# Kernel optimization log

Measured on AMD Instinct MI355X. Metric: run time of the kernel, lower is better.

Reference implementation:

```python
import jax, jax.numpy as jnp
import numpy as np

B, L, D = 1, 256, 256
H, DK, R = 8, 32, 2
EPS = 1e-6


def _proj_ode(x, t, W, b, r):
    """Stand-in for ODELinear/InterpLinear: linear projection of x broadcast
    over a second time index with r exponential time-decay coefficients.
    x: [B,L,D], t: [B,L] -> [B,L,L,r,D_out]"""
    base = x @ W.T + b                                  # [B,L,Do]
    dt = jnp.abs(t[:, :, None] - t[:, None, :])         # [B,L,L]
    steps = jnp.linspace(0.0, 1.0, r, dtype=x.dtype)    # [r]
    coef = jnp.exp(-dt[:, :, :, None] * steps)          # [B,L,L,r]
    return coef[..., None] * base[:, None, :, None, :]  # [B,L,L,r,Do]


def _layer_norm(x, g, b):
    mu = x.mean(-1, keepdims=True)
    var = ((x - mu) ** 2).mean(-1, keepdims=True)
    return (x - mu) * jax.lax.rsqrt(var + EPS) * g + b


def setup_inputs() -> dict:
    key = jax.random.key(0)
    ks = jax.random.split(key, 12)
    s = 1.0 / np.sqrt(D)
    return {
        "q": jax.random.normal(ks[0], (B, L, D), jnp.float32),
        "k": jax.random.normal(ks[1], (B, L, D), jnp.float32),
        "v": jax.random.normal(ks[2], (B, L, D), jnp.float32),
        "t": jax.random.uniform(ks[3], (B, L), jnp.float32),
        "Wq": jax.random.normal(ks[4], (D, D), jnp.float32) * s,
        "bq": jnp.zeros((D,), jnp.float32),
        "Wk": jax.random.normal(ks[5], (D, D), jnp.float32) * s,
        "bk": jnp.zeros((D,), jnp.float32),
        "Wv": jax.random.normal(ks[6], (D, D), jnp.float32) * s,
        "bv": jnp.zeros((D,), jnp.float32),
        "fc_w": jax.random.normal(ks[7], (D, D), jnp.float32) * s,
        "fc_b": jnp.zeros((D,), jnp.float32),
        "ln_g": jnp.ones((D,), jnp.float32),
        "ln_b": jnp.zeros((D,), jnp.float32),
    }


def reference(q, k, v, t, Wq, bq, Wk, bk, Wv, bv, fc_w, fc_b, ln_g, ln_b):
    temp = DK ** 0.5
    residual = q
    qn = _layer_norm(q, ln_g, ln_b)  # normalize_before=True (only q)

    # [B,L,L,R,D] -> [B,L,L,R,H,DK] -> [B,H,L,L,R,DK]
    def to6(x):
        return x.reshape(B, L, L, R, H, DK).transpose(0, 4, 1, 2, 3, 5)

    qp = to6(_proj_ode(qn, t, Wq, bq, R))
    kp = to6(_proj_ode(k, t, Wk, bk, R))
    vp = to6(_proj_ode(v, t, Wv, bv, R))

    # attn = (q/temp * k).sum(-1).sum(-1): multiply-reduce over (R, DK), no matmul
    attn = jnp.einsum('bhijrd,bhijrd->bhij', qp, kp) / temp
    attn = jax.nn.softmax(attn, axis=-1)  # dropout=0 (eval)

    vs = vp.sum(axis=4)                                   # reduce R: [B,H,L,L,DK]
    out = jnp.einsum('bhij,bhijd->bhid', attn, vs)        # reduce second L
    out = out.transpose(0, 2, 1, 3).reshape(B, L, H * DK)
    out = out @ fc_w.T + fc_b
    out = out + residual
    return (out, attn)
```

## Files before the change

kernel.cpp:

```cpp
#include <hip/hip_runtime.h>
#include <math.h>


#define INV_TEMP 0.17677669529663687f

__device__ __forceinline__ void gemm_panel(
    const float* __restrict__ X, const float* __restrict__ W,
    const float* __restrict__ bias, const float* __restrict__ ln_g,
    const float* __restrict__ ln_b, float* __restrict__ out, const int mode) {
  __shared__ float As[256][36];
  __shared__ float Bs[256][36];
  __shared__ float Red[4][32][36];
  const int t = threadIdx.x;
  const int j0 = blockIdx.y << 5, o0 = blockIdx.x << 5;
  const int lr = t >> 3;
  const int cg = (t & 7) << 2;
  float4 xa[8], wb[8];
#pragma unroll
  for (int u = 0; u < 8; ++u) {
    xa[u] = *(const float4*)(X + ((j0 + lr) << 8) + (u << 5) + cg);
    wb[u] = *(const float4*)(W + ((o0 + lr) << 8) + (u << 5) + cg);
  }
  if (mode == 0) {
    float s = 0.f, s2 = 0.f;
#pragma unroll
    for (int u = 0; u < 8; ++u) {
      s  += xa[u].x + xa[u].y + xa[u].z + xa[u].w;
      s2 += xa[u].x * xa[u].x + xa[u].y * xa[u].y +
            xa[u].z * xa[u].z + xa[u].w * xa[u].w;
    }
#pragma unroll
    for (int off = 1; off < 8; off <<= 1) {
      s  += __shfl_xor(s, off);
      s2 += __shfl_xor(s2, off);
    }
    const float mu = s * 0.00390625f;
    const float rs = rsqrtf(s2 * 0.00390625f - mu * mu + 1e-6f);
#pragma unroll
    for (int u = 0; u < 8; ++u) {
      const float4 gv = *(const float4*)(ln_g + (u << 5) + cg);
      const float4 bv = *(const float4*)(ln_b + (u << 5) + cg);
      xa[u].x = (xa[u].x - mu) * rs * gv.x + bv.x;
      xa[u].y = (xa[u].y - mu) * rs * gv.y + bv.y;
      xa[u].z = (xa[u].z - mu) * rs * gv.z + bv.z;
      xa[u].w = (xa[u].w - mu) * rs * gv.w + bv.w;
    }
  }
#pragma unroll
  for (int u = 0; u < 8; ++u) {
    const int c = (u << 5) + cg;
    As[c + 0][lr] = xa[u].x; As[c + 1][lr] = xa[u].y;
    As[c + 2][lr] = xa[u].z; As[c + 3][lr] = xa[u].w;
    Bs[c + 0][lr] = wb[u].x; Bs[c + 1][lr] = wb[u].y;
    Bs[c + 2][lr] = wb[u].z; Bs[c + 3][lr] = wb[u].w;
  }
  __syncthreads();

  const int w = t >> 6, lane = t & 63;
  const int jb = (lane >> 3) << 2;
  const int ob = (lane & 7) << 2;
  const int kbase = w << 6;
  float acc[4][4] = {{0.f}};
#pragma unroll 8
  for (int kk = 0; kk < 64; ++kk) {
    const float4 av = *(const float4*)&As[kbase + kk][jb];
    const float4 bv = *(const float4*)&Bs[kbase + kk][ob];
    acc[0][0] = fmaf(av.x, bv.x, acc[0][0]);
    acc[0][1] = fmaf(av.x, bv.y, acc[0][1]);
    acc[0][2] = fmaf(av.x, bv.z, acc[0][2]);
    acc[0][3] = fmaf(av.x, bv.w, acc[0][3]);
    acc[1][0] = fmaf(av.y, bv.x, acc[1][0]);
    acc[1][1] = fmaf(av.y, bv.y, acc[1][1]);
    acc[1][2] = fmaf(av.y, bv.z, acc[1][2]);
    acc[1][3] = fmaf(av.y, bv.w, acc[1][3]);
    acc[2][0] = fmaf(av.z, bv.x, acc[2][0]);
    acc[2][1] = fmaf(av.z, bv.y, acc[2][1]);
    acc[2][2] = fmaf(av.z, bv.z, acc[2][2]);
    acc[2][3] = fmaf(av.z, bv.w, acc[2][3]);
    acc[3][0] = fmaf(av.w, bv.x, acc[3][0]);
    acc[3][1] = fmaf(av.w, bv.y, acc[3][1]);
    acc[3][2] = fmaf(av.w, bv.z, acc[3][2]);
    acc[3][3] = fmaf(av.w, bv.w, acc[3][3]);
  }
#pragma unroll
  for (int r = 0; r < 4; ++r)
    *(float4*)&Red[w][jb + r][ob] =
        make_float4(acc[r][0], acc[r][1], acc[r][2], acc[r][3]);
  __syncthreads();

  const int j = t >> 3, o4 = (t & 7) << 2;
  const float4 s0 = *(const float4*)&Red[0][j][o4];
  const float4 s1 = *(const float4*)&Red[1][j][o4];
  const float4 s2 = *(const float4*)&Red[2][j][o4];
  const float4 s3 = *(const float4*)&Red[3][j][o4];
  const float4 bv4 = *(const float4*)(bias + o0 + o4);
  float4 rs4;
  rs4.x = (s0.x + s1.x) + (s2.x + s3.x) + bv4.x;
  rs4.y = (s0.y + s1.y) + (s2.y + s3.y) + bv4.y;
  rs4.z = (s0.z + s1.z) + (s2.z + s3.z) + bv4.z;
  rs4.w = (s0.w + s1.w) + (s2.w + s3.w) + bv4.w;
  const int gj = j0 + j, go = o0 + o4;
  if (mode <= 1) {
    out[((go + 0) << 8) + gj] = rs4.x;
    out[((go + 1) << 8) + gj] = rs4.y;
    out[((go + 2) << 8) + gj] = rs4.z;
    out[((go + 3) << 8) + gj] = rs4.w;
  } else {
    *(float4*)(out + (gj << 8) + go) = rs4;
  }
}

__global__ __launch_bounds__(256) void mha_proj_gemm3(
    const float* __restrict__ q, const float* __restrict__ kin,
    const float* __restrict__ vin, const float* __restrict__ Wq,
    const float* __restrict__ bq, const float* __restrict__ Wk,
    const float* __restrict__ bk, const float* __restrict__ Wv,
    const float* __restrict__ bv, const float* __restrict__ ln_g,
    const float* __restrict__ ln_b, const float* __restrict__ fc_w,
    float* __restrict__ baseQT, float* __restrict__ baseKT,
    float* __restrict__ baseV, float* __restrict__ fc_wT,
    float* __restrict__ outz) {
  const int z = blockIdx.z;
  const int gid = ((z << 6) + (blockIdx.y << 3) + blockIdx.x) * 256 +
                  threadIdx.x;
  if (gid < 16384)
    ((float4*)outz)[gid] = make_float4(0.f, 0.f, 0.f, 0.f);
  {
    const int e = gid << 1;
    if (e < 65536) {
      const float2 v = *(const float2*)(fc_w + e);
      const int o = e >> 8, d = e & 255;
      fc_wT[(d << 8) + o] = v.x;
      fc_wT[((d + 1 < 256 ? d + 1 : d - 255) << 8) +
            (d + 1 < 256 ? o : o + 1)] = v.y;
    }
  }
  if (z == 0)
    gemm_panel(q, Wq, bq, ln_g, ln_b, baseQT, 0);
  else if (z == 1)
    gemm_panel(kin, Wk, bk, nullptr, nullptr, baseKT, 1);
  else
    gemm_panel(vin, Wv, bv, nullptr, nullptr, baseV, 2);
}

__global__ __launch_bounds__(512) void mha_attn_fc(
    const float* __restrict__ baseQT, const float* __restrict__ baseKT,
    const float* __restrict__ baseV, const float* __restrict__ tt,
    const float* __restrict__ fc_wT, const float* __restrict__ fc_b,
    const float* __restrict__ qres, float* __restrict__ attn_out,
    float* __restrict__ out) {
  const int h = blockIdx.y;
  const int i0 = blockIdx.x << 3;
  const int t = threadIdx.x;
  __shared__ float s_lds[256];
  __shared__ float P[8][256];
  __shared__ float ctx_lds[8][32];
  if (t < 256) {
    const float* qc = baseQT + (h << 13) + t;
    const float* kc = baseKT + (h << 13) + t;
    float acc = 0.f;
#pragma unroll
    for (int dk = 0; dk < 32; ++dk)
      acc = fmaf(qc[dk << 8], kc[dk << 8], acc);
    s_lds[t] = acc * INV_TEMP;
  }
  __syncthreads();

  const int w = t >> 6, lane = t & 63;
  const int i = i0 + w;
  const float ti = tt[i];
  const float4 tj = ((const float4*)tt)[lane];
  const float4 sv = ((const float4*)s_lds)[lane];
  const float e0 = __expf(-fabsf(ti - tj.x));
  const float e1 = __expf(-fabsf(ti - tj.y));
  const float e2 = __expf(-fabsf(ti - tj.z));
  const float e3 = __expf(-fabsf(ti - tj.w));
  const float sc0 = (1.f + e0 * e0) * sv.x;
  const float sc1 = (1.f + e1 * e1) * sv.y;
  const float sc2 = (1.f + e2 * e2) * sv.z;
  const float sc3 = (1.f + e3 * e3) * sv.w;
  float m = fmaxf(fmaxf(sc0, sc1), fmaxf(sc2, sc3));
#pragma unroll
  for (int off = 32; off; off >>= 1) m = fmaxf(m, __shfl_xor(m, off));
  float p0 = __expf(sc0 - m), p1 = __expf(sc1 - m);
  float p2 = __expf(sc2 - m), p3 = __expf(sc3 - m);
  float s = p0 + p1 + p2 + p3;
#pragma unroll
  for (int off = 32; off; off >>= 1) s += __shfl_xor(s, off);
  const float rinv = 1.f / s;
  p0 *= rinv; p1 *= rinv; p2 *= rinv; p3 *= rinv;
  ((float4*)(attn_out + (((h << 8) + i) << 8)))[lane] =
      make_float4(p0, p1, p2, p3);
  ((float4*)P[w])[lane] = make_float4(p0 * (1.f + e0), p1 * (1.f + e1),
                                      p2 * (1.f + e2), p3 * (1.f + e3));

  const int dk = lane & 31, half = lane >> 5;
  const float* Pr = P[w] + (half << 7);
  const float* Vp = baseV + (h << 5) + dk + (half << 15);
  float a0 = 0.f, a1 = 0.f, a2 = 0.f, a3 = 0.f;
#pragma unroll 4
  for (int jj = 0; jj < 128; jj += 4) {
    a0 = fmaf(Pr[jj + 0], Vp[(jj + 0) << 8], a0);
    a1 = fmaf(Pr[jj + 1], Vp[(jj + 1) << 8], a1);
    a2 = fmaf(Pr[jj + 2], Vp[(jj + 2) << 8], a2);
    a3 = fmaf(Pr[jj + 3], Vp[(jj + 3) << 8], a3);
  }
  float acc = (a0 + a1) + (a2 + a3);
  acc += __shfl_xor(acc, 32);
  if (half == 0) ctx_lds[w][dk] = acc;
  __syncthreads();

  const int oq = lane << 2;
  float4 c4[8];
#pragma unroll
  for (int u = 0; u < 8; ++u)
    c4[u] = *(const float4*)&ctx_lds[w][u << 2];
  const float* wt = fc_wT + (h << 13) + oq;
  float4 acc4 = make_float4(0.f, 0.f, 0.f, 0.f);
#pragma unroll
  for (int u = 0; u < 8; ++u) {
    const float4 cc = c4[u];
    const float4 w0 = *(const float4*)(wt + ((u << 2) + 0 << 8));
    const float4 w1 = *(const float4*)(wt + ((u << 2) + 1 << 8));
    const float4 w2 = *(const float4*)(wt + ((u << 2) + 2 << 8));
    const float4 w3 = *(const float4*)(wt + ((u << 2) + 3 << 8));
    acc4.x = fmaf(cc.x, w0.x, fmaf(cc.y, w1.x, fmaf(cc.z, w2.x, fmaf(cc.w, w3.x, acc4.x))));
    acc4.y = fmaf(cc.x, w0.y, fmaf(cc.y, w1.y, fmaf(cc.z, w2.y, fmaf(cc.w, w3.y, acc4.y))));
    acc4.z = fmaf(cc.x, w0.z, fmaf(cc.y, w1.z, fmaf(cc.z, w2.z, fmaf(cc.w, w3.z, acc4.z))));
    acc4.w = fmaf(cc.x, w0.w, fmaf(cc.y, w1.w, fmaf(cc.z, w2.w, fmaf(cc.w, w3.w, acc4.w))));
  }
  if (h == 0) {
    const float4 bb = *(const float4*)(fc_b + oq);
    const float4 rr = *(const float4*)(qres + (i << 8) + oq);
    acc4.x += bb.x + rr.x; acc4.y += bb.y + rr.y;
    acc4.z += bb.z + rr.z; acc4.w += bb.w + rr.w;
  }
  float* op = out + (i << 8) + oq;
  unsafeAtomicAdd(op + 0, acc4.x);
  unsafeAtomicAdd(op + 1, acc4.y);
  unsafeAtomicAdd(op + 2, acc4.z);
  unsafeAtomicAdd(op + 3, acc4.w);
}

extern "C" void kernel_launch(void* const* d_in, const int* in_sizes, int n_in,
                              void* d_out, int out_size, void* d_ws,
                              size_t ws_size, hipStream_t stream) {
  const float* q    = (const float*)d_in[0];
  const float* kin  = (const float*)d_in[1];
  const float* vin  = (const float*)d_in[2];
  const float* tt   = (const float*)d_in[3];
  const float* Wq   = (const float*)d_in[4];
  const float* bq   = (const float*)d_in[5];
  const float* Wk   = (const float*)d_in[6];
  const float* bk   = (const float*)d_in[7];
  const float* Wv   = (const float*)d_in[8];
  const float* bv   = (const float*)d_in[9];
  const float* fc_w = (const float*)d_in[10];
  const float* fc_b = (const float*)d_in[11];
  const float* ln_g = (const float*)d_in[12];
  const float* ln_b = (const float*)d_in[13];

  float* out  = (float*)d_out;
  float* attn = out + 65536;

  float* ws     = (float*)d_ws;
  float* baseQT = ws;
  float* baseKT = ws + 65536;
  float* baseV  = ws + 131072;
  float* fc_wT  = ws + 196608;

  hipLaunchKernelGGL(mha_proj_gemm3, dim3(8, 8, 3), dim3(256), 0, stream, q,
                     kin, vin, Wq, bq, Wk, bk, Wv, bv, ln_g, ln_b, fc_w,
                     baseQT, baseKT, baseV, fc_wT, out);
  hipLaunchKernelGGL(mha_attn_fc, dim3(32, 8), dim3(512), 0, stream, baseQT,
                     baseKT, baseV, tt, fc_wT, fc_b, q, attn, out);
}
```

Before: 103.1 us.

## Loop heads inside attention block and replace atomic FC accumulation with direct stores

The attention kernel now gives each block 4 query rows and loops over all 8 heads inside the block, instead of using one block per (head, 8-row) tile. Each block therefore holds the full 256-wide context per row and can finish the output projection with plain float4 stores. This removes the zero-initialisation of the output in the first kernel and the per-head atomic adds. The cost is only 64 blocks of 256 threads, so far fewer waves are in flight. Each block also recomputes the per-head score vectors for all 8 heads, and the head loop runs serially inside each block.

```diff
diff --git a/kernel.cpp b/kernel.cpp
--- a/kernel.cpp
+++ b/kernel.cpp
@@ -118,13 +118,10 @@
     const float* __restrict__ bv, const float* __restrict__ ln_g,
     const float* __restrict__ ln_b, const float* __restrict__ fc_w,
     float* __restrict__ baseQT, float* __restrict__ baseKT,
-    float* __restrict__ baseV, float* __restrict__ fc_wT,
-    float* __restrict__ outz) {
+    float* __restrict__ baseV, float* __restrict__ fc_wT) {
   const int z = blockIdx.z;
   const int gid = ((z << 6) + (blockIdx.y << 3) + blockIdx.x) * 256 +
                   threadIdx.x;
-  if (gid < 16384)
-    ((float4*)outz)[gid] = make_float4(0.f, 0.f, 0.f, 0.f);
   {
     const int e = gid << 1;
     if (e < 65536) {
@@ -143,26 +140,27 @@
     gemm_panel(vin, Wv, bv, nullptr, nullptr, baseV, 2);
 }
 
-__global__ __launch_bounds__(512) void mha_attn_fc(
+__global__ __launch_bounds__(256) void mha_attn_fc(
     const float* __restrict__ baseQT, const float* __restrict__ baseKT,
     const float* __restrict__ baseV, const float* __restrict__ tt,
     const float* __restrict__ fc_wT, const float* __restrict__ fc_b,
     const float* __restrict__ qres, float* __restrict__ attn_out,
     float* __restrict__ out) {
-  const int h = blockIdx.y;
-  const int i0 = blockIdx.x << 3;
+  const int i0 = blockIdx.x << 2;
   const int t = threadIdx.x;
-  __shared__ float s_lds[256];
-  __shared__ float P[8][256];
-  __shared__ float ctx_lds[8][32];
-  if (t < 256) {
+  __shared__ float s_lds[8][256];
+  __shared__ float P[4][256];
+  __shared__ float ctx_lds[4][256];
+
+#pragma unroll
+  for (int h = 0; h < 8; ++h) {
     const float* qc = baseQT + (h << 13) + t;
     const float* kc = baseKT + (h << 13) + t;
     float acc = 0.f;
 #pragma unroll
     for (int dk = 0; dk < 32; ++dk)
       acc = fmaf(qc[dk << 8], kc[dk << 8], acc);
-    s_lds[t] = acc * INV_TEMP;
+    s_lds[h][t] = acc * INV_TEMP;
   }
   __syncthreads();
 
@@ -170,76 +168,62 @@
   const int i = i0 + w;
   const float ti = tt[i];
   const float4 tj = ((const float4*)tt)[lane];
-  const float4 sv = ((const float4*)s_lds)[lane];
   const float e0 = __expf(-fabsf(ti - tj.x));
   const float e1 = __expf(-fabsf(ti - tj.y));
   const float e2 = __expf(-fabsf(ti - tj.z));
   const float e3 = __expf(-fabsf(ti - tj.w));
-  const float sc0 = (1.f + e0 * e0) * sv.x;
-  const float sc1 = (1.f + e1 * e1) * sv.y;
-  const float sc2 = (1.f + e2 * e2) * sv.z;
-  const float sc3 = (1.f + e3 * e3) * sv.w;
-  float m = fmaxf(fmaxf(sc0, sc1), fmaxf(sc2, sc3));
-#pragma unroll
-  for (int off = 32; off; off >>= 1) m = fmaxf(m, __shfl_xor(m, off));
-  float p0 = __expf(sc0 - m), p1 = __expf(sc1 - m);
-  float p2 = __expf(sc2 - m), p3 = __expf(sc3 - m);
-  float s = p0 + p1 + p2 + p3;
-#pragma unroll
-  for (int off = 32; off; off >>= 1) s += __shfl_xor(s, off);
-  const float rinv = 1.f / s;
-  p0 *= rinv; p1 *= rinv; p2 *= rinv; p3 *= rinv;
-  ((float4*)(attn_out + (((h << 8) + i) << 8)))[lane] =
-      make_float4(p0, p1, p2, p3);
-  ((float4*)P[w])[lane] = make_float4(p0 * (1.f + e0), p1 * (1.f + e1),
-                                      p2 * (1.f + e2), p3 * (1.f + e3));
-
+  const float f0 = 1.f + e0, f1 = 1.f + e1, f2 = 1.f + e2, f3 = 1.f + e3;
+  const float g0 = 1.f + e0 * e0, g1 = 1.f + e1 * e1;
+  const float g2 = 1.f + e2 * e2, g3 = 1.f + e3 * e3;
   const int dk = lane & 31, half = lane >> 5;
-  const float* Pr = P[w] + (half << 7);
-  const float* Vp = baseV + (h << 5) + dk + (half << 15);
-  float a0 = 0.f, a1 = 0.f, a2 = 0.f, a3 = 0.f;
+
+  for (int h = 0; h < 8; ++h) {
+    const float4 sv = ((const float4*)s_lds[h])[lane];
+    const float sc0 = g0 * sv.x, sc1 = g1 * sv.y;
+    const float sc2 = g2 * sv.z, sc3 = g3 * sv.w;
+    float m = fmaxf(fmaxf(sc0, sc1), fmaxf(sc2, sc3));
+#pragma unroll
+    for (int off = 32; off; off >>= 1) m = fmaxf(m, __shfl_xor(m, off));
+    float p0 = __expf(sc0 - m), p1 = __expf(sc1 - m);
+    float p2 = __expf(sc2 - m), p3 = __expf(sc3 - m);
+    float s = p0 + p1 + p2 + p3;
+#pragma unroll
+    for (int off = 32; off; off >>= 1) s += __shfl_xor(s, off);
+    const float rinv = 1.f / s;
+    p0 *= rinv; p1 *= rinv; p2 *= rinv; p3 *= rinv;
+    ((float4*)(attn_out + (((h << 8) + i) << 8)))[lane] =
+        make_float4(p0, p1, p2, p3);
+    ((float4*)P[w])[lane] =
+        make_float4(p0 * f0, p1 * f1, p2 * f2, p3 * f3);
+    const float* Pr = P[w] + (half << 7);
+    const float* Vp = baseV + (h << 5) + dk + (half << 15);
+    float a0 = 0.f, a1 = 0.f, a2 = 0.f, a3 = 0.f;
 #pragma unroll 4
-  for (int jj = 0; jj < 128; jj += 4) {
-    a0 = fmaf(Pr[jj + 0], Vp[(jj + 0) << 8], a0);
-    a1 = fmaf(Pr[jj + 1], Vp[(jj + 1) << 8], a1);
-    a2 = fmaf(Pr[jj + 2], Vp[(jj + 2) << 8], a2);
-    a3 = fmaf(Pr[jj + 3], Vp[(jj + 3) << 8], a3);
-  }
-  float acc = (a0 + a1) + (a2 + a3);
-  acc += __shfl_xor(acc, 32);
-  if (half == 0) ctx_lds[w][dk] = acc;
-  __syncthreads();
+    for (int jj = 0; jj < 128; jj += 4) {
+      a0 = fmaf(Pr[jj + 0], Vp[(jj + 0) << 8], a0);
+      a1 = fmaf(Pr[jj + 1], Vp[(jj + 1) << 8], a1);
+      a2 = fmaf(Pr[jj + 2], Vp[(jj + 2) << 8], a2);
+      a3 = fmaf(Pr[jj + 3], Vp[(jj + 3) << 8], a3);
+    }
+    float acc = (a0 + a1) + (a2 + a3);
+    acc += __shfl_xor(acc, 32);
+    if (half == 0) ctx_lds[w][(h << 5) + dk] = acc;
+  }
 
   const int oq = lane << 2;
-  float4 c4[8];
-#pragma unroll
-  for (int u = 0; u < 8; ++u)
-    c4[u] = *(const float4*)&ctx_lds[w][u << 2];
-  const float* wt = fc_wT + (h << 13) + oq;
-  float4 acc4 = make_float4(0.f, 0.f, 0.f, 0.f);
-#pragma unroll
-  for (int u = 0; u < 8; ++u) {
-    const float4 cc = c4[u];
-    const float4 w0 = *(const float4*)(wt + ((u << 2) + 0 << 8));
-    const float4 w1 = *(const float4*)(wt + ((u << 2) + 1 << 8));
-    const float4 w2 = *(const float4*)(wt + ((u << 2) + 2 << 8));
-    const float4 w3 = *(const float4*)(wt + ((u << 2) + 3 << 8));
-    acc4.x = fmaf(cc.x, w0.x, fmaf(cc.y, w1.x, fmaf(cc.z, w2.x, fmaf(cc.w, w3.x, acc4.x))));
-    acc4.y = fmaf(cc.x, w0.y, fmaf(cc.y, w1.y, fmaf(cc.z, w2.y, fmaf(cc.w, w3.y, acc4.y))));
-    acc4.z = fmaf(cc.x, w0.z, fmaf(cc.y, w1.z, fmaf(cc.z, w2.z, fmaf(cc.w, w3.z, acc4.z))));
-    acc4.w = fmaf(cc.x, w0.w, fmaf(cc.y, w1.w, fmaf(cc.z, w2.w, fmaf(cc.w, w3.w, acc4.w))));
-  }
-  if (h == 0) {
-    const float4 bb = *(const float4*)(fc_b + oq);
-    const float4 rr = *(const float4*)(qres + (i << 8) + oq);
-    acc4.x += bb.x + rr.x; acc4.y += bb.y + rr.y;
-    acc4.z += bb.z + rr.z; acc4.w += bb.w + rr.w;
-  }
-  float* op = out + (i << 8) + oq;
-  unsafeAtomicAdd(op + 0, acc4.x);
-  unsafeAtomicAdd(op + 1, acc4.y);
-  unsafeAtomicAdd(op + 2, acc4.z);
-  unsafeAtomicAdd(op + 3, acc4.w);
+  const float4 bb = *(const float4*)(fc_b + oq);
+  const float4 rr = *(const float4*)(qres + (i << 8) + oq);
+  float4 acc4 = make_float4(bb.x + rr.x, bb.y + rr.y, bb.z + rr.z, bb.w + rr.w);
+#pragma unroll 4
+  for (int d = 0; d < 256; ++d) {
+    const float c = ctx_lds[w][d];
+    const float4 w4 = *(const float4*)(fc_wT + (d << 8) + oq);
+    acc4.x = fmaf(c, w4.x, acc4.x);
+    acc4.y = fmaf(c, w4.y, acc4.y);
+    acc4.z = fmaf(c, w4.z, acc4.z);
+    acc4.w = fmaf(c, w4.w, acc4.w);
+  }
+  *(float4*)(out + (i << 8) + oq) = acc4;
 }
 
 extern "C" void kernel_launch(void* const* d_in, const int* in_sizes, int n_in,
@@ -271,7 +255,7 @@
 
   hipLaunchKernelGGL(mha_proj_gemm3, dim3(8, 8, 3), dim3(256), 0, stream, q,
                      kin, vin, Wq, bq, Wk, bk, Wv, bv, ln_g, ln_b, fc_w,
-                     baseQT, baseKT, baseV, fc_wT, out);
-  hipLaunchKernelGGL(mha_attn_fc, dim3(32, 8), dim3(512), 0, stream, baseQT,
+                     baseQT, baseKT, baseV, fc_wT);
+  hipLaunchKernelGGL(mha_attn_fc, dim3(64), dim3(256), 0, stream, baseQT,
                      baseKT, baseV, tt, fc_wT, fc_b, q, attn, out);
 }
```

Measured after the change: 136.8 us. 32.7% more time.
